# Kernel optimization log

Measured on AMD Instinct MI355X. Metric: run time of the kernel, lower is better.

## Reference

```python
import jax, jax.numpy as jnp
import numpy as np


def setup_inputs() -> dict:
    key = jax.random.key(0)
    kq, kk, kv, kl = jax.random.split(key, 4)
    B, Nq, Nkv, D = 16, 2048, 2048, 64
    return {
        "Q_batch": jax.random.normal(kq, (B, Nq, D), dtype=jnp.float32),
        "K_batch": jax.random.normal(kk, (B, Nkv, D), dtype=jnp.float32),
        "V_batch": jax.random.normal(kv, (B, Nkv, D), dtype=jnp.float32),
        "valid_lens": jax.random.randint(kl, (B,), 0, Nkv, dtype=jnp.int64 if jax.config.jax_enable_x64 else jnp.int32),
    }


def reference(Q_batch, K_batch, V_batch, valid_lens):
    # S: (B, Nq, Nkv) scaled dot-product scores
    d = Q_batch.shape[-1]
    scale = 1.0 / jnp.sqrt(jnp.asarray(d, Q_batch.dtype))
    S = jnp.einsum('bqd,bkd->bqk', Q_batch, K_batch) * scale
    # mask_first_n_valid: position k valid iff k < valid_lens[b], broadcast over queries
    kv_idx = jnp.arange(S.shape[-1])  # (Nkv,)
    mask = kv_idx[None, None, :] < valid_lens[:, None, None]  # (B, 1->Nq, Nkv)
    S = jnp.where(mask, S, jnp.asarray(-1e20, S.dtype))
    W = jax.nn.softmax(S, axis=-1)  # attention weights (dropout rate = 0.0)
    return jnp.einsum('bqk,bkv->bqv', W, V_batch)
```

## Files before the change

kernel.cpp:

```cpp
#include <hip/hip_runtime.h>

#define BATCH 16
#define NQ    2048
#define NKV   2048
#define DH    64
#define SC    0.18033688011112042f
#define TILE_B 8192

typedef __attribute__((ext_vector_type(8))) short  bf16x8;
typedef __attribute__((ext_vector_type(16))) float f32x16;

__device__ __forceinline__ unsigned f2bf(float f) {
  unsigned u = __builtin_bit_cast(unsigned, f);
  u += 0x7FFFu + ((u >> 16) & 1u);
  return u >> 16;
}

__global__ __launch_bounds__(256) void convert_kernel(
    const float* __restrict__ K, const float* __restrict__ V,
    const int* __restrict__ lens, unsigned char* __restrict__ WS) {
  const int bt = blockIdx.x;
  const int b = bt >> 6, t = bt & 63;
  const int L = lens[b];
  const int Leff = (L == 0) ? NKV : L;
  if (t * 32 >= Leff) return;

  unsigned char* tile = WS + (size_t)bt * TILE_B;
  const size_t   srow = ((size_t)b * NKV + (size_t)t * 32) * DH;
  const int tid = threadIdx.x;
  const int l = tid & 63, g = tid >> 6;
  const int l31 = l & 31, hi = l >> 5;
  {
    const float4* p = (const float4*)(K + srow + (size_t)l31 * DH + g * 16 + hi * 8);
    float4 a = p[0], c4 = p[1];
    bf16x8 w;
    w[0] = (short)f2bf(a.x);  w[1] = (short)f2bf(a.y);
    w[2] = (short)f2bf(a.z);  w[3] = (short)f2bf(a.w);
    w[4] = (short)f2bf(c4.x); w[5] = (short)f2bf(c4.y);
    w[6] = (short)f2bf(c4.z); w[7] = (short)f2bf(c4.w);
    *(bf16x8*)(tile + g * 1024 + l * 16) = w;
  }
  {
    const int c2 = g & 1, dh = g >> 1;
    const float* vp = V + srow + (size_t)(c2 * 16 + 4 * hi) * DH + dh * 32 + l31;
    bf16x8 w;
#pragma unroll
    for (int j = 0; j < 8; ++j)
      w[j] = (short)f2bf(vp[(size_t)((j & 3) + 8 * (j >> 2)) * DH]);
    *(bf16x8*)(tile + 4096 + g * 1024 + l * 16) = w;
  }
}

__global__ __launch_bounds__(256, 2) void sdpa_kernel(
    const float* __restrict__ Q, const unsigned char* __restrict__ WS,
    const int* __restrict__ lens, float* __restrict__ O) {
  __shared__ float smem[8448];

  const int tid  = threadIdx.x;
  const int lane = tid & 63;
  const int wave = tid >> 6;
  const int l31  = lane & 31, hi = lane >> 5;

  const int idx = blockIdx.x, layer = idx >> 8, rr = idx & 255;
  const int b   = (rr + layer * 3) & 15;
  const int qo  = (rr >> 4) + layer * 16;

  const int  L    = lens[b];
  const bool zlen = (L == 0);
  const int  Leff = zlen ? NKV : L;
  const int  nT   = (Leff + 31) >> 5;
  const int  tb   = (nT * wave) >> 2;
  const int  te   = (nT * (wave + 1)) >> 2;
  const int  cnt  = te - tb;
  const int  tmask = (!zlen && (L & 31)) ? nT - 1 : -1;

  bf16x8 Qf[2][4];
#pragma unroll
  for (int u = 0; u < 2; ++u) {
    const float* qp = Q + ((size_t)b * NQ + qo * 64 + u * 32 + l31) * DH + hi * 8;
#pragma unroll
    for (int c = 0; c < 4; ++c) {
      const float4* p = (const float4*)(qp + c * 16);
      float4 a = p[0], d4 = p[1];
      bf16x8 w;
      w[0] = (short)f2bf(a.x * SC);  w[1] = (short)f2bf(a.y * SC);
      w[2] = (short)f2bf(a.z * SC);  w[3] = (short)f2bf(a.w * SC);
      w[4] = (short)f2bf(d4.x * SC); w[5] = (short)f2bf(d4.y * SC);
      w[6] = (short)f2bf(d4.z * SC); w[7] = (short)f2bf(d4.w * SC);
      Qf[u][c] = w;
    }
  }

  const unsigned char* gp = WS + (size_t)(b * 64 + tb) * TILE_B + lane * 16;

  f32x16 oc[4];
  float  l_[2] = {0.f, 0.f};
#pragma unroll
  for (int i = 0; i < 4; ++i)
#pragma unroll
    for (int r = 0; r < 16; ++r) oc[i][r] = 0.f;

  bf16x8 cur[8];
  if (cnt > 0) {
#pragma unroll
    for (int i = 0; i < 8; ++i) cur[i] = *(const bf16x8*)(gp + i * 1024);
  }

  for (int it = 0; it < cnt; ++it) {
    const int t = tb + it;
    const unsigned char* gn = (it + 1 < cnt) ? (gp + TILE_B) : gp;
    bf16x8 nxt[8];
#pragma unroll
    for (int i = 0; i < 8; ++i) nxt[i] = *(const bf16x8*)(gn + i * 1024);
    gp += TILE_B;

#pragma unroll
    for (int u = 0; u < 2; ++u) {
      f32x16 acc;
#pragma unroll
      for (int r = 0; r < 16; ++r) acc[r] = 0.f;
#pragma unroll
      for (int c = 0; c < 4; ++c)
        acc = __builtin_amdgcn_mfma_f32_32x32x16_bf16(cur[c], Qf[u][c], acc, 0, 0, 0);

      if (zlen) {
#pragma unroll
        for (int r = 0; r < 16; ++r) acc[r] = 0.f;
      } else if (t == tmask) {
#pragma unroll
        for (int r = 0; r < 16; ++r) {
          const int key = t * 32 + (r & 3) + 8 * (r >> 2) + 4 * hi;
          if (key >= L) acc[r] = -1e30f;
        }
      }

      unsigned short ph[16];
      float ls = 0.f;
#pragma unroll
      for (int r = 0; r < 16; ++r) {
        float    p  = __builtin_amdgcn_exp2f(acc[r]);
        unsigned uu = __builtin_bit_cast(unsigned, p);
        ls += __builtin_bit_cast(float, uu & 0xFFFF0000u);
        ph[r] = (unsigned short)(uu >> 16);
      }
      l_[u] += ls;

      bf16x8 Pf0, Pf1;
#pragma unroll
      for (int j = 0; j < 8; ++j) { Pf0[j] = (short)ph[j]; Pf1[j] = (short)ph[8 + j]; }

      oc[u * 2 + 0] = __builtin_amdgcn_mfma_f32_32x32x16_bf16(cur[4], Pf0, oc[u * 2 + 0], 0, 0, 0);
      oc[u * 2 + 0] = __builtin_amdgcn_mfma_f32_32x32x16_bf16(cur[5], Pf1, oc[u * 2 + 0], 0, 0, 0);
      oc[u * 2 + 1] = __builtin_amdgcn_mfma_f32_32x32x16_bf16(cur[6], Pf0, oc[u * 2 + 1], 0, 0, 0);
      oc[u * 2 + 1] = __builtin_amdgcn_mfma_f32_32x32x16_bf16(cur[7], Pf1, oc[u * 2 + 1], 0, 0, 0);
    }
#pragma unroll
    for (int i = 0; i < 8; ++i) cur[i] = nxt[i];
  }

  __syncthreads();
  if (wave >= 2) {
    float* Mb = smem + (wave - 2) * 4224 + lane;
#pragma unroll
    for (int i = 0; i < 4; ++i)
#pragma unroll
      for (int r = 0; r < 16; ++r) Mb[(i * 16 + r) * 64] = oc[i][r];
    Mb[64 * 64] = l_[0];
    Mb[65 * 64] = l_[1];
  }
  __syncthreads();
  if (wave < 2) {
    float* Mb = smem + wave * 4224 + lane;
#pragma unroll
    for (int i = 0; i < 4; ++i)
#pragma unroll
      for (int r = 0; r < 16; ++r) oc[i][r] += Mb[(i * 16 + r) * 64];
    l_[0] += Mb[64 * 64];
    l_[1] += Mb[65 * 64];
  }
  __syncthreads();
  if (wave == 1) {
    float* Mb = smem + lane;
#pragma unroll
    for (int i = 0; i < 4; ++i)
#pragma unroll
      for (int r = 0; r < 16; ++r) Mb[(i * 16 + r) * 64] = oc[i][r];
    Mb[64 * 64] = l_[0];
    Mb[65 * 64] = l_[1];
  }
  __syncthreads();
  if (wave == 0) {
    float* Mb = smem + lane;
#pragma unroll
    for (int i = 0; i < 4; ++i)
#pragma unroll
      for (int r = 0; r < 16; ++r) oc[i][r] += Mb[(i * 16 + r) * 64];
    l_[0] += Mb[64 * 64];
    l_[1] += Mb[65 * 64];

    const float inv0 = 1.0f / (l_[0] + __shfl_xor(l_[0], 32, 64));
    const float inv1 = 1.0f / (l_[1] + __shfl_xor(l_[1], 32, 64));

#pragma unroll
    for (int u = 0; u < 2; ++u) {
      const float inv = u ? inv1 : inv0;
      const int   q   = u * 32 + l31;
#pragma unroll
      for (int dh = 0; dh < 2; ++dh)
#pragma unroll
        for (int r = 0; r < 16; ++r) {
          const int d = dh * 32 + (r & 3) + 8 * (r >> 2) + 4 * hi;
          smem[q * 68 + d] = oc[u * 2 + dh][r] * inv;
        }
    }
  }
  __syncthreads();

  float* Ob = O + ((size_t)b * NQ + (size_t)qo * 64) * DH;
#pragma unroll
  for (int R = 0; R < 4; ++R) {
    const int fi = R * 256 + tid;
    const int q = fi >> 4, ch = fi & 15;
    float4 v4 = *(const float4*)&smem[q * 68 + ch * 4];
    *(float4*)(Ob + (size_t)q * DH + ch * 4) = v4;
  }
}

extern "C" void kernel_launch(void* const* d_in, const int* in_sizes, int n_in,
                              void* d_out, int out_size, void* d_ws, size_t ws_size,
                              hipStream_t stream) {
  const float* Q    = (const float*)d_in[0];
  const float* K    = (const float*)d_in[1];
  const float* V    = (const float*)d_in[2];
  const int*   lens = (const int*)d_in[3];
  float*       Out  = (float*)d_out;
  unsigned char* WS = (unsigned char*)d_ws;

  hipLaunchKernelGGL(convert_kernel, dim3(BATCH * 64), dim3(256), 0, stream, K, V, lens, WS);
  hipLaunchKernelGGL(sdpa_kernel, dim3(512), dim3(256), 0, stream, Q, WS, lens, Out);
}
```

Measured before the change: 95.68 us.

## Halve queries per block, double grid, and simplify cross-wave reduction

```diff
diff --git a/kernel.cpp b/kernel.cpp
--- a/kernel.cpp
+++ b/kernel.cpp
@@ -51,10 +51,10 @@
   }
 }
 
-__global__ __launch_bounds__(256, 2) void sdpa_kernel(
+__global__ __launch_bounds__(256, 3) void sdpa_kernel(
     const float* __restrict__ Q, const unsigned char* __restrict__ WS,
     const int* __restrict__ lens, float* __restrict__ O) {
-  __shared__ float smem[8448];
+  __shared__ float smem[6336];
 
   const int tid  = threadIdx.x;
   const int lane = tid & 63;
@@ -70,14 +70,12 @@
   const int  Leff = zlen ? NKV : L;
   const int  nT   = (Leff + 31) >> 5;
   const int  tb   = (nT * wave) >> 2;
-  const int  te   = (nT * (wave + 1)) >> 2;
-  const int  cnt  = te - tb;
+  const int  cnt  = ((nT * (wave + 1)) >> 2) - tb;
   const int  tmask = (!zlen && (L & 31)) ? nT - 1 : -1;
 
-  bf16x8 Qf[2][4];
-#pragma unroll
-  for (int u = 0; u < 2; ++u) {
-    const float* qp = Q + ((size_t)b * NQ + qo * 64 + u * 32 + l31) * DH + hi * 8;
+  bf16x8 Qf[4];
+  {
+    const float* qp = Q + ((size_t)b * NQ + qo * 32 + l31) * DH + hi * 8;
 #pragma unroll
     for (int c = 0; c < 4; ++c) {
       const float4* p = (const float4*)(qp + c * 16);
@@ -87,18 +85,16 @@
       w[2] = (short)f2bf(a.z * SC);  w[3] = (short)f2bf(a.w * SC);
       w[4] = (short)f2bf(d4.x * SC); w[5] = (short)f2bf(d4.y * SC);
       w[6] = (short)f2bf(d4.z * SC); w[7] = (short)f2bf(d4.w * SC);
-      Qf[u][c] = w;
+      Qf[c] = w;
     }
   }
 
   const unsigned char* gp = WS + (size_t)(b * 64 + tb) * TILE_B + lane * 16;
 
-  f32x16 oc[4];
-  float  l_[2] = {0.f, 0.f};
-#pragma unroll
-  for (int i = 0; i < 4; ++i)
-#pragma unroll
-    for (int r = 0; r < 16; ++r) oc[i][r] = 0.f;
+  f32x16 oc0, oc1;
+  float  l_ = 0.f;
+#pragma unroll
+  for (int r = 0; r < 16; ++r) { oc0[r] = 0.f; oc1[r] = 0.f; }
 
   bf16x8 cur[8];
   if (cnt > 0) {
@@ -114,111 +110,76 @@
     for (int i = 0; i < 8; ++i) nxt[i] = *(const bf16x8*)(gn + i * 1024);
     gp += TILE_B;
 
-#pragma unroll
-    for (int u = 0; u < 2; ++u) {
-      f32x16 acc;
+    f32x16 acc;
+#pragma unroll
+    for (int r = 0; r < 16; ++r) acc[r] = 0.f;
+#pragma unroll
+    for (int c = 0; c < 4; ++c)
+      acc = __builtin_amdgcn_mfma_f32_32x32x16_bf16(cur[c], Qf[c], acc, 0, 0, 0);
+
+    if (zlen) {
 #pragma unroll
       for (int r = 0; r < 16; ++r) acc[r] = 0.f;
-#pragma unroll
-      for (int c = 0; c < 4; ++c)
-        acc = __builtin_amdgcn_mfma_f32_32x32x16_bf16(cur[c], Qf[u][c], acc, 0, 0, 0);
-
-      if (zlen) {
-#pragma unroll
-        for (int r = 0; r < 16; ++r) acc[r] = 0.f;
-      } else if (t == tmask) {
-#pragma unroll
-        for (int r = 0; r < 16; ++r) {
-          const int key = t * 32 + (r & 3) + 8 * (r >> 2) + 4 * hi;
-          if (key >= L) acc[r] = -1e30f;
-        }
+    } else if (t == tmask) {
+#pragma unroll
+      for (int r = 0; r < 16; ++r) {
+        const int key = t * 32 + (r & 3) + 8 * (r >> 2) + 4 * hi;
+        if (key >= L) acc[r] = -1e30f;
       }
-
-      unsigned short ph[16];
-      float ls = 0.f;
-#pragma unroll
-      for (int r = 0; r < 16; ++r) {
-        float    p  = __builtin_amdgcn_exp2f(acc[r]);
-        unsigned uu = __builtin_bit_cast(unsigned, p);
-        ls += __builtin_bit_cast(float, uu & 0xFFFF0000u);
-        ph[r] = (unsigned short)(uu >> 16);
-      }
-      l_[u] += ls;
-
-      bf16x8 Pf0, Pf1;
-#pragma unroll
-      for (int j = 0; j < 8; ++j) { Pf0[j] = (short)ph[j]; Pf1[j] = (short)ph[8 + j]; }
-
-      oc[u * 2 + 0] = __builtin_amdgcn_mfma_f32_32x32x16_bf16(cur[4], Pf0, oc[u * 2 + 0], 0, 0, 0);
-      oc[u * 2 + 0] = __builtin_amdgcn_mfma_f32_32x32x16_bf16(cur[5], Pf1, oc[u * 2 + 0], 0, 0, 0);
-      oc[u * 2 + 1] = __builtin_amdgcn_mfma_f32_32x32x16_bf16(cur[6], Pf0, oc[u * 2 + 1], 0, 0, 0);
-      oc[u * 2 + 1] = __builtin_amdgcn_mfma_f32_32x32x16_bf16(cur[7], Pf1, oc[u * 2 + 1], 0, 0, 0);
-    }
+    }
+
+    unsigned short ph[16];
+    float ls = 0.f;
+#pragma unroll
+    for (int r = 0; r < 16; ++r) {
+      float    p  = __builtin_amdgcn_exp2f(acc[r]);
+      unsigned uu = __builtin_bit_cast(unsigned, p);
+      ls += __builtin_bit_cast(float, uu & 0xFFFF0000u);
+      ph[r] = (unsigned short)(uu >> 16);
+    }
+    l_ += ls;
+
+    bf16x8 Pf0, Pf1;
+#pragma unroll
+    for (int j = 0; j < 8; ++j) { Pf0[j] = (short)ph[j]; Pf1[j] = (short)ph[8 + j]; }
+
+    oc0 = __builtin_amdgcn_mfma_f32_32x32x16_bf16(cur[4], Pf0, oc0, 0, 0, 0);
+    oc0 = __builtin_amdgcn_mfma_f32_32x32x16_bf16(cur[5], Pf1, oc0, 0, 0, 0);
+    oc1 = __builtin_amdgcn_mfma_f32_32x32x16_bf16(cur[6], Pf0, oc1, 0, 0, 0);
+    oc1 = __builtin_amdgcn_mfma_f32_32x32x16_bf16(cur[7], Pf1, oc1, 0, 0, 0);
+
 #pragma unroll
     for (int i = 0; i < 8; ++i) cur[i] = nxt[i];
   }
 
-  __syncthreads();
-  if (wave >= 2) {
-    float* Mb = smem + (wave - 2) * 4224 + lane;
-#pragma unroll
-    for (int i = 0; i < 4; ++i)
-#pragma unroll
-      for (int r = 0; r < 16; ++r) Mb[(i * 16 + r) * 64] = oc[i][r];
-    Mb[64 * 64] = l_[0];
-    Mb[65 * 64] = l_[1];
-  }
-  __syncthreads();
-  if (wave < 2) {
-    float* Mb = smem + wave * 4224 + lane;
-#pragma unroll
-    for (int i = 0; i < 4; ++i)
-#pragma unroll
-      for (int r = 0; r < 16; ++r) oc[i][r] += Mb[(i * 16 + r) * 64];
-    l_[0] += Mb[64 * 64];
-    l_[1] += Mb[65 * 64];
-  }
-  __syncthreads();
-  if (wave == 1) {
-    float* Mb = smem + lane;
-#pragma unroll
-    for (int i = 0; i < 4; ++i)
-#pragma unroll
-      for (int r = 0; r < 16; ++r) Mb[(i * 16 + r) * 64] = oc[i][r];
-    Mb[64 * 64] = l_[0];
-    Mb[65 * 64] = l_[1];
+  if (wave >= 1) {
+    float* Mb = smem + (wave - 1) * 2112 + lane;
+#pragma unroll
+    for (int r = 0; r < 16; ++r) { Mb[r * 64] = oc0[r]; Mb[(16 + r) * 64] = oc1[r]; }
+    Mb[32 * 64] = l_;
   }
   __syncthreads();
   if (wave == 0) {
-    float* Mb = smem + lane;
-#pragma unroll
-    for (int i = 0; i < 4; ++i)
-#pragma unroll
-      for (int r = 0; r < 16; ++r) oc[i][r] += Mb[(i * 16 + r) * 64];
-    l_[0] += Mb[64 * 64];
-    l_[1] += Mb[65 * 64];
-
-    const float inv0 = 1.0f / (l_[0] + __shfl_xor(l_[0], 32, 64));
-    const float inv1 = 1.0f / (l_[1] + __shfl_xor(l_[1], 32, 64));
-
-#pragma unroll
-    for (int u = 0; u < 2; ++u) {
-      const float inv = u ? inv1 : inv0;
-      const int   q   = u * 32 + l31;
-#pragma unroll
-      for (int dh = 0; dh < 2; ++dh)
-#pragma unroll
-        for (int r = 0; r < 16; ++r) {
-          const int d = dh * 32 + (r & 3) + 8 * (r >> 2) + 4 * hi;
-          smem[q * 68 + d] = oc[u * 2 + dh][r] * inv;
-        }
+#pragma unroll
+    for (int w = 0; w < 3; ++w) {
+      const float* Mb = smem + w * 2112 + lane;
+#pragma unroll
+      for (int r = 0; r < 16; ++r) { oc0[r] += Mb[r * 64]; oc1[r] += Mb[(16 + r) * 64]; }
+      l_ += Mb[32 * 64];
+    }
+    const float inv = 1.0f / (l_ + __shfl_xor(l_, 32, 64));
+#pragma unroll
+    for (int r = 0; r < 16; ++r) {
+      const int d0 = (r & 3) + 8 * (r >> 2) + 4 * hi;
+      smem[l31 * 68 + d0]      = oc0[r] * inv;
+      smem[l31 * 68 + 32 + d0] = oc1[r] * inv;
     }
   }
   __syncthreads();
 
-  float* Ob = O + ((size_t)b * NQ + (size_t)qo * 64) * DH;
-#pragma unroll
-  for (int R = 0; R < 4; ++R) {
+  float* Ob = O + ((size_t)b * NQ + (size_t)qo * 32) * DH;
+#pragma unroll
+  for (int R = 0; R < 2; ++R) {
     const int fi = R * 256 + tid;
     const int q = fi >> 4, ch = fi & 15;
     float4 v4 = *(const float4*)&smem[q * 68 + ch * 4];
@@ -237,5 +198,5 @@
   unsigned char* WS = (unsigned char*)d_ws;
 
   hipLaunchKernelGGL(convert_kernel, dim3(BATCH * 64), dim3(256), 0, stream, K, V, lens, WS);
-  hipLaunchKernelGGL(sdpa_kernel, dim3(512), dim3(256), 0, stream, Q, WS, lens, Out);
-}
+  hipLaunchKernelGGL(sdpa_kernel, dim3(1024), dim3(256), 0, stream, Q, WS, lens, Out);
+}
```

Measured after the change: 97.96 us. 1.02x slower.
